# Performance work log

Measured on AMD Instinct MI355X. Metric: run time of the kernel, lower is better.

The kernel has to match this reference:

```python
import jax, jax.numpy as jnp
import numpy as np

IMG = 224          # image_size
FMAP = (56, 56)    # feature_map_dims (AdaptiveAvgPool2d((56,56)))
K_REWEIGHT = 3     # self.n_reweight
BLUR_RADIUS = 4    # KNNGaussianBlur(4): kernel 9, sigma 4


def _cdist(a, b):
    # Euclidean pairwise distance, [Na, D] x [Nb, D] -> [Na, Nb]
    a2 = jnp.sum(a * a, axis=1, keepdims=True)            # [Na,1]
    b2 = jnp.sum(b * b, axis=1, keepdims=True).T          # [1,Nb]
    d2 = a2 + b2 - 2.0 * (a @ b.T)
    return jnp.sqrt(jnp.maximum(d2, 0.0))


def _gaussian_blur(x):
    # x: [1,1,H,W]; torchvision GaussianBlur(kernel=9, sigma=4), reflect pad
    r, sigma = BLUR_RADIUS, float(BLUR_RADIUS)
    t = jnp.arange(2 * r + 1, dtype=x.dtype) - r
    g = jnp.exp(-(t * t) / (2.0 * sigma * sigma))
    g = g / jnp.sum(g)
    k2d = jnp.outer(g, g)[None, None]                     # [1,1,9,9]
    xp = jnp.pad(x, ((0, 0), (0, 0), (r, r), (r, r)), mode='reflect')
    return jax.lax.conv_general_dilated(
        xp, k2d, window_strides=(1, 1), padding='VALID',
        dimension_numbers=('NCHW', 'OIHW', 'NCHW'))


def setup_inputs() -> dict:
    key = jax.random.key(0)
    k1, k2 = jax.random.split(key)
    patch = jax.random.normal(k1, (FMAP[0] * FMAP[1], 768), dtype=jnp.float32)
    patch_lib = jax.random.normal(k2, (16384, 768), dtype=jnp.float32)
    mean = jnp.zeros((), dtype=jnp.float32)
    std = jnp.ones((), dtype=jnp.float32)
    return {"patch": patch, "patch_lib": patch_lib, "mean": mean, "std": std}


def reference(patch, patch_lib, mean, std):
    # normalization (method_name != 'Point_MAE' branch)
    p = (patch - mean) / std                               # [N, D]

    dist = _cdist(p, patch_lib)                            # [N, Nlib]
    min_val = jnp.min(dist, axis=1)                        # [N]
    min_idx = jnp.argmin(dist, axis=1)                     # [N]
    s_idx = jnp.argmax(min_val)
    s_star = jnp.max(min_val)

    m_test = p[s_idx]                                      # [D]
    m_star = patch_lib[min_idx[s_idx]]                     # [D]

    # distances of m_star to whole bank, k smallest
    w_dist = jnp.sqrt(jnp.maximum(
        jnp.sum((patch_lib - m_star) ** 2, axis=1), 0.0))  # [Nlib]
    _, nn_idx = jax.lax.top_k(-w_dist, K_REWEIGHT)         # smallest k
    m_star_knn = jnp.linalg.norm(
        m_test[None, :] - patch_lib[nn_idx[1:]], axis=1)   # [k-1]

    D_sqrt = jnp.sqrt(jnp.asarray(patch.shape[1], dtype=p.dtype))
    w = 1.0 - jnp.exp(s_star / D_sqrt) / jnp.sum(jnp.exp(m_star_knn / D_sqrt))
    s = w * s_star

    s_map = min_val.reshape(1, 1, *FMAP)
    s_map = jax.image.resize(s_map, (1, 1, IMG, IMG), method='bilinear')
    s_map = _gaussian_blur(s_map)
    return s, s_map
```

## Files before the change

kernel.cpp:

```cpp
#include <hip/hip_runtime.h>
#include <hip/hip_bf16.h>
#include <stdint.h>

#define N_PATCH 3136
#define N_PATCH_PAD 3328
#define N_LIB   16384
#define DIM     768
#define IMGSZ   224
#define FM      56

#define TILE 256
#define KT2 12
#define MT 13
#define NTILES 64

#define TAILB 64
#define D2_MARGIN 8.0f

typedef __bf16 bf16_t;
typedef __bf16 bf16x8 __attribute__((ext_vector_type(8)));
typedef __bf16 bf16x4_v __attribute__((ext_vector_type(4)));
typedef float  f32x4  __attribute__((ext_vector_type(4)));

#define FLT_MAX_ 3.402823466e+38f

#define BARF() do { asm volatile("" ::: "memory"); \
                    __builtin_amdgcn_s_barrier();  \
                    asm volatile("" ::: "memory"); } while (0)

struct Scal {
  unsigned long long approx_max_pack;
  unsigned long long cand_pack[64];
  int cand[64];
  int cand_count;
  int bar[4];
  int work;
};

__device__ __forceinline__ float wave_reduce_sum(float v) {
#pragma unroll
  for (int s = 32; s > 0; s >>= 1) v += __shfl_xor(v, s, 64);
  return v;
}

__device__ __forceinline__ float wave_reduce_min(float v) {
#pragma unroll
  for (int s = 32; s > 0; s >>= 1) v = fminf(v, __shfl_xor(v, s, 64));
  return v;
}

__device__ __forceinline__ unsigned long long shfl_xor_u64(unsigned long long v, int mask) {
  unsigned lo = (unsigned)v, hi = (unsigned)(v >> 32);
  lo = __shfl_xor(lo, mask, 64);
  hi = __shfl_xor(hi, mask, 64);
  return ((unsigned long long)hi << 32) | lo;
}

__device__ __forceinline__ void async16(const bf16_t* g, bf16_t* l) {
  __builtin_amdgcn_global_load_lds(
      (const __attribute__((address_space(1))) unsigned int*)g,
      (__attribute__((address_space(3))) unsigned int*)l, 16, 0, 0);
}

__device__ __forceinline__ void grid_bar(int* ctr, int nb) {
  __syncthreads();
  if (threadIdx.x == 0) {
    __threadfence();
    atomicAdd(ctr, 1);
    while (atomicAdd(ctr, 0) < nb) __builtin_amdgcn_s_sleep(8);
    __threadfence();
  }
  __syncthreads();
}

__device__ __forceinline__ float bf16u_to_f(unsigned short u) {
  return __uint_as_float(((unsigned)u) << 16);
}

__global__ void prep_kernel(const float* __restrict__ patch, const float* __restrict__ lib,
                            const float* __restrict__ meanp, const float* __restrict__ stdp,
                            bf16_t* __restrict__ pb, bf16_t* __restrict__ lb,
                            float* __restrict__ a2, float* __restrict__ b2, Scal* sc) {
  int t = threadIdx.x;
  int lane = t & 63;
  if (blockIdx.x == 0) {
    if (t < 64) sc->cand_pack[t] = ~0ULL;
    if (t == 64) { sc->approx_max_pack = 0ULL; sc->cand_count = 0; }
    if (t >= 65 && t < 69) sc->bar[t - 65] = 0;
    if (t == 69) sc->work = 0;
  }
  if (blockIdx.x < N_PATCH_PAD / 4) {
    int row = blockIdx.x * 4 + (t >> 6);
    if (row < N_PATCH) {
      float mu = meanp[0], sd = stdp[0];
      float acc = 0.f;
#pragma unroll
      for (int k = 0; k < 3; k++) {
        float4 v = ((const float4*)(patch + (size_t)row * DIM))[lane + 64 * k];
        v.x = (v.x - mu) / sd; v.y = (v.y - mu) / sd;
        v.z = (v.z - mu) / sd; v.w = (v.w - mu) / sd;
        bf16x4_v o = {(__bf16)v.x, (__bf16)v.y, (__bf16)v.z, (__bf16)v.w};
        *(bf16x4_v*)(pb + (size_t)row * DIM + (lane + 64 * k) * 4) = o;
        acc += v.x*v.x + v.y*v.y + v.z*v.z + v.w*v.w;
      }
      acc = wave_reduce_sum(acc);
      if (lane == 0) a2[row] = acc;
    } else {
      bf16x4_v z = {(__bf16)0.f, (__bf16)0.f, (__bf16)0.f, (__bf16)0.f};
#pragma unroll
      for (int k = 0; k < 3; k++)
        *(bf16x4_v*)(pb + (size_t)row * DIM + (lane + 64 * k) * 4) = z;
    }
  } else {
    int row = (blockIdx.x - N_PATCH_PAD / 4) * 4 + (t >> 6);
    float acc = 0.f;
#pragma unroll
    for (int k = 0; k < 3; k++) {
      float4 v = ((const float4*)(lib + (size_t)row * DIM))[lane + 64 * k];
      bf16x4_v o = {(__bf16)v.x, (__bf16)v.y, (__bf16)v.z, (__bf16)v.w};
      *(bf16x4_v*)(lb + (size_t)row * DIM + (lane + 64 * k) * 4) = o;
      acc += v.x*v.x + v.y*v.y + v.z*v.z + v.w*v.w;
    }
    acc = wave_reduce_sum(acc);
    if (lane == 0) b2[row] = acc;
  }
}

__global__ __launch_bounds__(512, 2)
void gemm_min_kernel(const bf16_t* __restrict__ pb, const bf16_t* __restrict__ lb,
                     const float* __restrict__ a2, const float* __restrict__ b2,
                     float* __restrict__ part) {
  __shared__ __align__(16) bf16_t As[2][2][128 * 64];
  __shared__ __align__(16) bf16_t Bs[2][2][128 * 64];

  const int t = threadIdx.x;
  const int wave = t >> 6;
  const int lane = t & 63;
  const int l15 = lane & 15;
  const int quad = lane >> 4;
  const int wm = (wave >> 2) * 128;
  const int wn = (wave & 3) * 64;
  const int mhw = wm >> 7;
  const int nhw = wn >> 7;
  const int wni = wn & 64;

  const int L0 = t >> 3;
  const int k0 = (t & 7) ^ (L0 & 7);
  const int sl0 = (((0 * 4 + quad) ^ (l15 & 7)) << 4);
  const int sl1 = (((1 * 4 + quad) ^ (l15 & 7)) << 4);

  const int x = blockIdx.x & 7;
  const int sblk = blockIdx.x >> 3;
  const int nt = x * 8 + (sblk & 7);
  const int n0 = nt * TILE;

  for (int g = 0; g < 4; ++g) {
    if (g * 32 + sblk >= 104) break;
    const int mt = g * 4 + (sblk >> 3);
    const int m0 = mt * TILE;

    __syncthreads();

    const bf16_t* gA = pb + (size_t)(m0 + L0) * DIM + k0 * 8;
    const bf16_t* gB = lb + (size_t)(n0 + L0) * DIM + k0 * 8;

    auto stageA = [&](int tk, int mh) {
      bf16_t* dst = &As[tk & 1][mh][0];
      const bf16_t* s = gA + (size_t)(mh * 128) * DIM + tk * 64;
      async16(s, dst + t * 8);
      async16(s + (size_t)64 * DIM, dst + 4096 + t * 8);
    };
    auto stageB = [&](int tk, int nh) {
      bf16_t* dst = &Bs[tk & 1][nh][0];
      const bf16_t* s = gB + (size_t)(nh * 128) * DIM + tk * 64;
      async16(s, dst + t * 8);
      async16(s + (size_t)64 * DIM, dst + 4096 + t * 8);
    };

    f32x4 acc[8][4];
#pragma unroll
    for (int mi = 0; mi < 8; mi++)
#pragma unroll
      for (int ni = 0; ni < 4; ni++) { f32x4 z = {0.f,0.f,0.f,0.f}; acc[mi][ni] = z; }

    bf16x8 afr[4][2], bf[2][2];

    auto readA = [&](int d, int mh) {
      const char* base = (const char*)&As[d][mhw][0];
#pragma unroll
      for (int mi = 0; mi < 4; mi++) {
        int lr = mh * 64 + mi * 16 + l15;
        afr[mi][0] = *(const bf16x8*)(base + lr * 128 + sl0);
        afr[mi][1] = *(const bf16x8*)(base + lr * 128 + sl1);
      }
    };
    auto readB = [&](int d, int nh) {
      const char* base = (const char*)&Bs[d][nhw][0];
#pragma unroll
      for (int ni = 0; ni < 2; ni++) {
        int lr = wni + nh * 32 + ni * 16 + l15;
        bf[ni][0] = *(const bf16x8*)(base + lr * 128 + sl0);
        bf[ni][1] = *(const bf16x8*)(base + lr * 128 + sl1);
      }
    };
    auto mfq = [&](int mh, int nh) {
      __builtin_amdgcn_s_setprio(1);
#pragma unroll
      for (int mi = 0; mi < 4; mi++)
#pragma unroll
        for (int ni = 0; ni < 2; ni++) {
          acc[mh*4+mi][nh*2+ni] = __builtin_amdgcn_mfma_f32_16x16x32_bf16(
              afr[mi][0], bf[ni][0], acc[mh*4+mi][nh*2+ni], 0, 0, 0);
          acc[mh*4+mi][nh*2+ni] = __builtin_amdgcn_mfma_f32_16x16x32_bf16(
              afr[mi][1], bf[ni][1], acc[mh*4+mi][nh*2+ni], 0, 0, 0);
        }
      __builtin_amdgcn_s_setprio(0);
    };

    auto half_iter = [&](int d, int tst, bool stg) {
      if (stg) {
        stageA(tst, 0);
        asm volatile("s_waitcnt vmcnt(2)" ::: "memory");
      } else {
        asm volatile("s_waitcnt vmcnt(0)" ::: "memory");
      }
      BARF();
      readB(d, 0);
      readA(d, 0);
      mfq(0, 0);
      BARF();
      readB(d, 1);
      if (stg) { stageA(tst, 1); stageB(tst, 0); }
      BARF();
      mfq(0, 1);
      BARF();
      readA(d, 1);
      if (stg) stageB(tst, 1);
      BARF();
      mfq(1, 1);
      BARF();
      readB(d, 0);
      BARF();
      mfq(1, 0);
      BARF();
    };

    stageA(0, 0); stageA(0, 1); stageB(0, 0); stageB(0, 1);

    for (int tt = 0; tt < 10; tt += 2) {
      half_iter(0, tt + 1, true);
      half_iter(1, tt + 2, true);
    }
    half_iter(0, 11, true);
    half_iter(1, 12, false);

    __syncthreads();
    unsigned* smin = (unsigned*)&As[0][0][0];
    if (t < 256) smin[t] = 0xffffffffu;
    __syncthreads();

    float b2n[4];
#pragma unroll
    for (int ni = 0; ni < 4; ni++) b2n[ni] = b2[n0 + wn + ni * 16 + l15];

#pragma unroll
    for (int mi = 0; mi < 8; mi++) {
#pragma unroll
      for (int r = 0; r < 4; r++) {
        int rloc = wm + mi * 16 + quad * 4 + r;
        int mrow = m0 + rloc;
        float a2v = a2[mrow < N_PATCH ? mrow : (N_PATCH - 1)];
        float best = a2v + b2n[0] - 2.0f * acc[mi][0][r];
#pragma unroll
        for (int ni = 1; ni < 4; ni++)
          best = fminf(best, a2v + b2n[ni] - 2.0f * acc[mi][ni][r]);
        best = fmaxf(best, 0.0f);
#pragma unroll
        for (int s = 1; s < 16; s <<= 1)
          best = fminf(best, __shfl_xor(best, s, 64));
        if (l15 == 0) atomicMin(&smin[rloc], __float_as_uint(best));
      }
    }
    __syncthreads();
    if (t < 256) part[(size_t)nt * N_PATCH_PAD + m0 + t] = __uint_as_float(smin[t]);
  }
}

__device__ __forceinline__ void wave_pick(const Scal* sc, int cnt, int lane,
                                          int* srow, float* sstar, int* ms) {
  unsigned long long pk = 0ULL;
  int rowv = 0, msv = 0;
  if (lane < cnt) {
    unsigned long long cp = sc->cand_pack[lane];
    rowv = sc->cand[lane];
    msv = (int)(cp & 0xffffffffu);
    pk = (cp & 0xffffffff00000000ULL) | (unsigned)(0xffffffffu - (unsigned)rowv);
  }
  unsigned long long m = pk;
#pragma unroll
  for (int s = 1; s < 64; s <<= 1) {
    unsigned long long o = shfl_xor_u64(m, s);
    if (o > m) m = o;
  }
  unsigned long long mask = __ballot(pk == m && lane < cnt);
  int wl = (int)(__ffsll((long long)mask) - 1);
  *srow = __shfl(rowv, wl, 64);
  *ms   = __shfl(msv, wl, 64);
  *sstar = sqrtf(__uint_as_float((unsigned)(m >> 32)));
}

__global__ __launch_bounds__(256, 2)
void tail_kernel(const float* __restrict__ part, float* __restrict__ min_val,
                 const float* __restrict__ patch, const float* __restrict__ lib,
                 const bf16_t* __restrict__ lb,
                 const float* __restrict__ meanp, const float* __restrict__ stdp,
                 Scal* __restrict__ sc, float* __restrict__ wdist2,
                 float* __restrict__ out0, float* __restrict__ outmap) {
  __shared__ union {
    unsigned long long sl[768];
    float rs[40 * 40];
  } sm;
  __shared__ float redbuf[4];
  __shared__ unsigned long long rb64[4];
  __shared__ int s_cnt;

  const int t = threadIdx.x;
  const int b = blockIdx.x;
  const int wave = t >> 6, lane = t & 63;

  {
    int row = b * 256 + t;
    unsigned long long mp = 0ULL;
    if (row < N_PATCH) {
      float m = FLT_MAX_;
#pragma unroll 8
      for (int nt = 0; nt < NTILES; nt++)
        m = fminf(m, part[(size_t)nt * N_PATCH_PAD + row]);
      float v = sqrtf(m);
      min_val[row] = v;
      mp = (((unsigned long long)__float_as_uint(v)) << 32) |
           (unsigned)(0xffffffffu - (unsigned)row);
    }
#pragma unroll
    for (int s = 1; s < 64; s <<= 1) {
      unsigned long long o = shfl_xor_u64(mp, s);
      if (o > mp) mp = o;
    }
    if (lane == 0) rb64[wave] = mp;
    __syncthreads();
    if (t == 0) {
      unsigned long long mm = rb64[0];
      if (rb64[1] > mm) mm = rb64[1];
      if (rb64[2] > mm) mm = rb64[2];
      if (rb64[3] > mm) mm = rb64[3];
      if (mm) atomicMax(&sc->approx_max_pack, mm);
    }
  }
  grid_bar(&sc->bar[0], TAILB);

  if (b == 0) {
    float amax = __uint_as_float((unsigned)(atomicMax(&sc->approx_max_pack, 0ULL) >> 32));
    for (int i = t; i < N_PATCH; i += 256) {
      if (min_val[i] >= amax - 0.05f) {
        int p = atomicAdd(&sc->cand_count, 1);
        if (p < 64) sc->cand[p] = i;
      }
    }
  }
  grid_bar(&sc->bar[1], TAILB);

  if (t == 0) s_cnt = atomicAdd(&sc->cand_count, 0);
  __syncthreads();
  int cnt = s_cnt; if (cnt > 64) cnt = 64;

  {
    float mu = meanp[0], sd = stdp[0];
    for (int c = 0; c < cnt; c++) {
      int row = sc->cand[c];
      float pv_ = (t < NTILES) ? part[(size_t)t * N_PATCH_PAD + row] : FLT_MAX_;
      pv_ = wave_reduce_min(pv_);
      if (lane == 0) redbuf[wave] = pv_;
      __syncthreads();
      float bmin = fminf(fminf(redbuf[0], redbuf[1]), fminf(redbuf[2], redbuf[3]));
      __syncthreads();

      float4 pv[3];
#pragma unroll
      for (int k = 0; k < 3; k++) {
        float4 v = ((const float4*)(patch + (size_t)row * DIM))[lane + 64 * k];
        v.x = (v.x - mu) / sd; v.y = (v.y - mu) / sd;
        v.z = (v.z - mu) / sd; v.w = (v.w - mu) / sd;
        pv[k] = v;
      }
      int nt = b;
      float pmin = part[(size_t)nt * N_PATCH_PAD + row];
      if (pmin <= bmin + D2_MARGIN) {
        unsigned long long best = ~0ULL;
        int jb = nt * 256 + wave * 64;
        for (int rr = 0; rr < 64; rr++) {
          int j = jb + rr;
          const float4* pl = (const float4*)(lib + (size_t)j * DIM);
          float acc = 0.f;
#pragma unroll
          for (int k = 0; k < 3; k++) {
            float4 l = pl[lane + 64 * k];
            float dx = pv[k].x - l.x, dy = pv[k].y - l.y;
            float dz = pv[k].z - l.z, dw = pv[k].w - l.w;
            acc += dx*dx + dy*dy + dz*dz + dw*dw;
          }
          acc = wave_reduce_sum(acc);
          unsigned long long pk = (((unsigned long long)__float_as_uint(acc)) << 32) | (unsigned)j;
          if (pk < best) best = pk;
        }
        if (lane == 0) atomicMin(&sc->cand_pack[c], best);
      }
    }
  }
  grid_bar(&sc->bar[2], TAILB);

  {
    int srow_, ms; float ss_;
    wave_pick(sc, cnt, lane, &srow_, &ss_, &ms);
    float pm[12];
    const ushort4* pms = (const ushort4*)(lb + (size_t)ms * DIM);
#pragma unroll
    for (int k = 0; k < 3; k++) {
      ushort4 u = pms[lane + 64 * k];
      pm[k*4+0] = bf16u_to_f(u.x); pm[k*4+1] = bf16u_to_f(u.y);
      pm[k*4+2] = bf16u_to_f(u.z); pm[k*4+3] = bf16u_to_f(u.w);
    }
    int jbase = b * 256 + wave * 64;
    for (int rr = 0; rr < 64; rr += 2) {
      int j0 = jbase + rr, j1 = j0 + 1;
      const ushort4* r0 = (const ushort4*)(lb + (size_t)j0 * DIM);
      const ushort4* r1 = (const ushort4*)(lb + (size_t)j1 * DIM);
      float a0 = 0.f, a1 = 0.f;
#pragma unroll
      for (int k = 0; k < 3; k++) {
        ushort4 u0 = r0[lane + 64 * k];
        ushort4 u1 = r1[lane + 64 * k];
        float d;
        d = bf16u_to_f(u0.x) - pm[k*4+0]; a0 += d * d;
        d = bf16u_to_f(u0.y) - pm[k*4+1]; a0 += d * d;
        d = bf16u_to_f(u0.z) - pm[k*4+2]; a0 += d * d;
        d = bf16u_to_f(u0.w) - pm[k*4+3]; a0 += d * d;
        d = bf16u_to_f(u1.x) - pm[k*4+0]; a1 += d * d;
        d = bf16u_to_f(u1.y) - pm[k*4+1]; a1 += d * d;
        d = bf16u_to_f(u1.z) - pm[k*4+2]; a1 += d * d;
        d = bf16u_to_f(u1.w) - pm[k*4+3]; a1 += d * d;
      }
      a0 = wave_reduce_sum(a0);
      a1 = wave_reduce_sum(a1);
      if (lane == 0) { wdist2[j0] = a0; wdist2[j1] = a1; }
    }
  }
  grid_bar(&sc->bar[3], TAILB);

  if (b == 0) {
    unsigned long long b0 = ~0ULL, b1 = ~0ULL, b2 = ~0ULL;
    for (int j = t; j < N_LIB; j += 256) {
      unsigned long long pk = (((unsigned long long)__float_as_uint(wdist2[j])) << 32) | (unsigned)j;
      if (pk < b0)      { b2 = b1; b1 = b0; b0 = pk; }
      else if (pk < b1) { b2 = b1; b1 = pk; }
      else if (pk < b2) { b2 = pk; }
    }
    sm.sl[t * 3 + 0] = b0; sm.sl[t * 3 + 1] = b1; sm.sl[t * 3 + 2] = b2;
    __syncthreads();
    if (t >= 64) return;

    unsigned long long c0 = ~0ULL, c1 = ~0ULL, c2 = ~0ULL;
#pragma unroll
    for (int e = 0; e < 12; e++) {
      unsigned long long pk = sm.sl[t * 12 + e];
      if (pk < c0)      { c2 = c1; c1 = c0; c0 = pk; }
      else if (pk < c1) { c2 = c1; c1 = pk; }
      else if (pk < c2) { c2 = pk; }
    }
    unsigned long long res1 = 0, res2 = 0;
#pragma unroll
    for (int r = 0; r < 3; r++) {
      unsigned long long m = c0;
#pragma unroll
      for (int s = 1; s < 64; s <<= 1) {
        unsigned long long o = shfl_xor_u64(m, s);
        if (o < m) m = o;
      }
      if (r == 1) res1 = m;
      if (r == 2) res2 = m;
      if (c0 == m) { c0 = c1; c1 = c2; c2 = ~0ULL; }
    }
    int nA = (int)(res1 & 0xffffffffu);
    int nB = (int)(res2 & 0xffffffffu);

    int srow, ms2; float sstar;
    wave_pick(sc, cnt, t, &srow, &sstar, &ms2);

    float mu = meanp[0], sd = stdp[0];
    float accA = 0.f, accB = 0.f;
#pragma unroll
    for (int k = 0; k < 3; k++) {
      float4 p4 = ((const float4*)(patch + (size_t)srow * DIM))[t + 64 * k];
      float4 a4 = ((const float4*)(lib + (size_t)nA * DIM))[t + 64 * k];
      float4 b4 = ((const float4*)(lib + (size_t)nB * DIM))[t + 64 * k];
      float px = (p4.x - mu) / sd, py = (p4.y - mu) / sd;
      float pz = (p4.z - mu) / sd, pw = (p4.w - mu) / sd;
      float dax = px - a4.x, day = py - a4.y, daz = pz - a4.z, daw = pw - a4.w;
      float dbx = px - b4.x, dby = py - b4.y, dbz = pz - b4.z, dbw = pw - b4.w;
      accA += dax*dax + day*day + daz*daz + daw*daw;
      accB += dbx*dbx + dby*dby + dbz*dbz + dbw*dbw;
    }
    accA = wave_reduce_sum(accA);
    accB = wave_reduce_sum(accB);
    if (t == 0) {
      float dsq = sqrtf((float)DIM);
      float d1 = sqrtf(accA), d2v = sqrtf(accB);
      float w = 1.0f - expf(sstar / dsq) / (expf(d1 / dsq) + expf(d2v / dsq));
      out0[0] = w * sstar;
    }
    return;
  }

  if (b > 49) return;
  {
    int tile = b - 1;
    int bx = tile % 7, by = tile / 7;
    int ox0 = bx * 32, oy0 = by * 32;

    for (int i = t; i < 1600; i += 256) {
      int ly = i / 40, lx = i % 40;
      int gy = oy0 - 4 + ly; gy = gy < 0 ? 0 : (gy > 223 ? 223 : gy);
      int gx = ox0 - 4 + lx; gx = gx < 0 ? 0 : (gx > 223 ? 223 : gx);
      float sy = fminf(fmaxf(0.25f * gy - 0.375f, 0.0f), 55.0f);
      float sx = fminf(fmaxf(0.25f * gx - 0.375f, 0.0f), 55.0f);
      int y0 = (int)sy; if (y0 > 54) y0 = 54;
      int x0 = (int)sx; if (x0 > 54) x0 = 54;
      float fy = sy - y0, fx = sx - x0;
      float v00 = min_val[y0*FM + x0],     v01 = min_val[y0*FM + x0 + 1];
      float v10 = min_val[(y0+1)*FM + x0], v11 = min_val[(y0+1)*FM + x0 + 1];
      float a = v00 + fx * (v01 - v00);
      float bb = v10 + fx * (v11 - v10);
      sm.rs[i] = a + fy * (bb - a);
    }
    __syncthreads();

    float g[9]; float gs = 0.f;
#pragma unroll
    for (int i = 0; i < 9; i++) { float tt = (float)(i - 4); g[i] = expf(-(tt*tt)/32.0f); gs += g[i]; }
#pragma unroll
    for (int i = 0; i < 9; i++) g[i] /= gs;

    for (int p = t; p < 1024; p += 256) {
      int y = oy0 + p / 32, x = ox0 + (p & 31);
      float acc = 0.f;
#pragma unroll
      for (int dy = 0; dy < 9; dy++) {
        int yy = y + dy - 4;
        yy = yy < 0 ? -yy : (yy > IMGSZ - 1 ? 2*(IMGSZ-1) - yy : yy);
        int lyy = yy - (oy0 - 4);
        float ra = 0.f;
#pragma unroll
        for (int dx = 0; dx < 9; dx++) {
          int xx = x + dx - 4;
          xx = xx < 0 ? -xx : (xx > IMGSZ - 1 ? 2*(IMGSZ-1) - xx : xx);
          ra += g[dx] * sm.rs[lyy * 40 + (xx - (ox0 - 4))];
        }
        acc += g[dy] * ra;
      }
      outmap[y * IMGSZ + x] = acc;
    }
  }
}

extern "C" void kernel_launch(void* const* d_in, const int* in_sizes, int n_in,
                              void* d_out, int out_size, void* d_ws, size_t ws_size,
                              hipStream_t stream) {
  const float* patch = (const float*)d_in[0];
  const float* lib   = (const float*)d_in[1];
  const float* meanp = (const float*)d_in[2];
  const float* stdp  = (const float*)d_in[3];
  float* out = (float*)d_out;

  char* ws = (char*)d_ws;
  size_t off = 0;
  auto alloc = [&](size_t bytes) -> void* {
    void* p = ws + off;
    off = (off + bytes + 255) & ~(size_t)255;
    return p;
  };
  bf16_t* pb      = (bf16_t*)alloc((size_t)N_PATCH_PAD * DIM * sizeof(bf16_t));
  bf16_t* lb      = (bf16_t*)alloc((size_t)N_LIB * DIM * sizeof(bf16_t));
  float* a2       = (float*)alloc(N_PATCH * sizeof(float));
  float* b2       = (float*)alloc(N_LIB * sizeof(float));
  float* part     = (float*)alloc((size_t)N_PATCH_PAD * NTILES * sizeof(float));
  float* min_val  = (float*)alloc(N_PATCH * sizeof(float));
  float* wdist2   = (float*)alloc(N_LIB * sizeof(float));
  Scal*  sc       = (Scal*)alloc(sizeof(Scal));

  prep_kernel<<<N_PATCH_PAD / 4 + N_LIB / 4, 256, 0, stream>>>(patch, lib, meanp, stdp,
                                                               pb, lb, a2, b2, sc);
  gemm_min_kernel<<<256, 512, 0, stream>>>(pb, lb, a2, b2, part);
  tail_kernel<<<TAILB, 256, 0, stream>>>(part, min_val, patch, lib, lb, meanp, stdp,
                                         sc, wdist2, out, out + 1);
}
```

Measured before the change: 329.5 us.

## Simplify GEMM main loop to one-barrier double buffering and transpose partial-min layout

Replaces the fine-grained interleaved half-iteration schedule, which had many barriers and staged A/B halves between MFMA quarters, with a simple loop. Each k-tile now does a full wait and one barrier, issues the next tile's async loads, then computes the whole tile with B fragments held in registers. The per-tile partial minimum buffer is transposed to row-major [row][tile], so the tail reduction reads 64 contiguous values per row with one wave per row. The full vmcnt(0) wait per iteration may expose more load latency than the old staggered schedule did, and holding more fragments in registers raises register pressure.

```diff
diff --git a/kernel.cpp b/kernel.cpp
--- a/kernel.cpp
+++ b/kernel.cpp
@@ -23,10 +23,6 @@
 typedef float  f32x4  __attribute__((ext_vector_type(4)));
 
 #define FLT_MAX_ 3.402823466e+38f
-
-#define BARF() do { asm volatile("" ::: "memory"); \
-                    __builtin_amdgcn_s_barrier();  \
-                    asm volatile("" ::: "memory"); } while (0)
 
 struct Scal {
   unsigned long long approx_max_pack;
@@ -164,95 +160,70 @@
     const bf16_t* gA = pb + (size_t)(m0 + L0) * DIM + k0 * 8;
     const bf16_t* gB = lb + (size_t)(n0 + L0) * DIM + k0 * 8;
 
-    auto stageA = [&](int tk, int mh) {
-      bf16_t* dst = &As[tk & 1][mh][0];
-      const bf16_t* s = gA + (size_t)(mh * 128) * DIM + tk * 64;
-      async16(s, dst + t * 8);
-      async16(s + (size_t)64 * DIM, dst + 4096 + t * 8);
+    auto stageT = [&](int tk) {
+      bf16_t* dA0 = &As[tk & 1][0][0];
+      bf16_t* dA1 = &As[tk & 1][1][0];
+      bf16_t* dB0 = &Bs[tk & 1][0][0];
+      bf16_t* dB1 = &Bs[tk & 1][1][0];
+      const bf16_t* sA = gA + tk * 64;
+      const bf16_t* sB = gB + tk * 64;
+      async16(sA,                       dA0 + t * 8);
+      async16(sA + (size_t)64  * DIM,   dA0 + 4096 + t * 8);
+      async16(sA + (size_t)128 * DIM,   dA1 + t * 8);
+      async16(sA + (size_t)192 * DIM,   dA1 + 4096 + t * 8);
+      async16(sB,                       dB0 + t * 8);
+      async16(sB + (size_t)64  * DIM,   dB0 + 4096 + t * 8);
+      async16(sB + (size_t)128 * DIM,   dB1 + t * 8);
+      async16(sB + (size_t)192 * DIM,   dB1 + 4096 + t * 8);
     };
-    auto stageB = [&](int tk, int nh) {
-      bf16_t* dst = &Bs[tk & 1][nh][0];
-      const bf16_t* s = gB + (size_t)(nh * 128) * DIM + tk * 64;
-      async16(s, dst + t * 8);
-      async16(s + (size_t)64 * DIM, dst + 4096 + t * 8);
+
+    f32x4 acc[8][4];
+#pragma unroll
+    for (int mi = 0; mi < 8; mi++)
+#pragma unroll
+      for (int ni = 0; ni < 4; ni++) { f32x4 z = {0.f,0.f,0.f,0.f}; acc[mi][ni] = z; }
+
+    auto computeTile = [&](int d) {
+      const char* Ab = (const char*)&As[d][mhw][0];
+      const char* Bb = (const char*)&Bs[d][nhw][0];
+      bf16x8 bfr[4][2];
+#pragma unroll
+      for (int ni = 0; ni < 4; ni++) {
+        int lr = wni + ni * 16 + l15;
+        bfr[ni][0] = *(const bf16x8*)(Bb + lr * 128 + sl0);
+        bfr[ni][1] = *(const bf16x8*)(Bb + lr * 128 + sl1);
+      }
+#pragma unroll
+      for (int q = 0; q < 4; q++) {
+        bf16x8 aq[2][2];
+#pragma unroll
+        for (int mi = 0; mi < 2; mi++) {
+          int lr = q * 32 + mi * 16 + l15;
+          aq[mi][0] = *(const bf16x8*)(Ab + lr * 128 + sl0);
+          aq[mi][1] = *(const bf16x8*)(Ab + lr * 128 + sl1);
+        }
+        __builtin_amdgcn_s_setprio(1);
+#pragma unroll
+        for (int mi = 0; mi < 2; mi++)
+#pragma unroll
+          for (int ni = 0; ni < 4; ni++) {
+            acc[q*2+mi][ni] = __builtin_amdgcn_mfma_f32_16x16x32_bf16(
+                aq[mi][0], bfr[ni][0], acc[q*2+mi][ni], 0, 0, 0);
+            acc[q*2+mi][ni] = __builtin_amdgcn_mfma_f32_16x16x32_bf16(
+                aq[mi][1], bfr[ni][1], acc[q*2+mi][ni], 0, 0, 0);
+          }
+        __builtin_amdgcn_s_setprio(0);
+      }
     };
 
-    f32x4 acc[8][4];
-#pragma unroll
-    for (int mi = 0; mi < 8; mi++)
-#pragma unroll
-      for (int ni = 0; ni < 4; ni++) { f32x4 z = {0.f,0.f,0.f,0.f}; acc[mi][ni] = z; }
-
-    bf16x8 afr[4][2], bf[2][2];
-
-    auto readA = [&](int d, int mh) {
-      const char* base = (const char*)&As[d][mhw][0];
-#pragma unroll
-      for (int mi = 0; mi < 4; mi++) {
-        int lr = mh * 64 + mi * 16 + l15;
-        afr[mi][0] = *(const bf16x8*)(base + lr * 128 + sl0);
-        afr[mi][1] = *(const bf16x8*)(base + lr * 128 + sl1);
-      }
-    };
-    auto readB = [&](int d, int nh) {
-      const char* base = (const char*)&Bs[d][nhw][0];
-#pragma unroll
-      for (int ni = 0; ni < 2; ni++) {
-        int lr = wni + nh * 32 + ni * 16 + l15;
-        bf[ni][0] = *(const bf16x8*)(base + lr * 128 + sl0);
-        bf[ni][1] = *(const bf16x8*)(base + lr * 128 + sl1);
-      }
-    };
-    auto mfq = [&](int mh, int nh) {
-      __builtin_amdgcn_s_setprio(1);
-#pragma unroll
-      for (int mi = 0; mi < 4; mi++)
-#pragma unroll
-        for (int ni = 0; ni < 2; ni++) {
-          acc[mh*4+mi][nh*2+ni] = __builtin_amdgcn_mfma_f32_16x16x32_bf16(
-              afr[mi][0], bf[ni][0], acc[mh*4+mi][nh*2+ni], 0, 0, 0);
-          acc[mh*4+mi][nh*2+ni] = __builtin_amdgcn_mfma_f32_16x16x32_bf16(
-              afr[mi][1], bf[ni][1], acc[mh*4+mi][nh*2+ni], 0, 0, 0);
-        }
-      __builtin_amdgcn_s_setprio(0);
-    };
-
-    auto half_iter = [&](int d, int tst, bool stg) {
-      if (stg) {
-        stageA(tst, 0);
-        asm volatile("s_waitcnt vmcnt(2)" ::: "memory");
-      } else {
-        asm volatile("s_waitcnt vmcnt(0)" ::: "memory");
-      }
-      BARF();
-      readB(d, 0);
-      readA(d, 0);
-      mfq(0, 0);
-      BARF();
-      readB(d, 1);
-      if (stg) { stageA(tst, 1); stageB(tst, 0); }
-      BARF();
-      mfq(0, 1);
-      BARF();
-      readA(d, 1);
-      if (stg) stageB(tst, 1);
-      BARF();
-      mfq(1, 1);
-      BARF();
-      readB(d, 0);
-      BARF();
-      mfq(1, 0);
-      BARF();
-    };
-
-    stageA(0, 0); stageA(0, 1); stageB(0, 0); stageB(0, 1);
-
-    for (int tt = 0; tt < 10; tt += 2) {
-      half_iter(0, tt + 1, true);
-      half_iter(1, tt + 2, true);
-    }
-    half_iter(0, 11, true);
-    half_iter(1, 12, false);
+    stageT(0);
+    for (int tk = 0; tk < KT2; ++tk) {
+      asm volatile("s_waitcnt vmcnt(0) lgkmcnt(0)" ::: "memory");
+      __builtin_amdgcn_s_barrier();
+      asm volatile("" ::: "memory");
+      if (tk + 1 < KT2) stageT(tk + 1);
+      computeTile(tk & 1);
+    }
 
     __syncthreads();
     unsigned* smin = (unsigned*)&As[0][0][0];
@@ -282,7 +253,7 @@
       }
     }
     __syncthreads();
-    if (t < 256) part[(size_t)nt * N_PATCH_PAD + m0 + t] = __uint_as_float(smin[t]);
+    if (t < 256) part[(size_t)(m0 + t) * NTILES + nt] = __uint_as_float(smin[t]);
   }
 }
 
@@ -329,22 +300,19 @@
   const int wave = t >> 6, lane = t & 63;
 
   {
-    int row = b * 256 + t;
     unsigned long long mp = 0ULL;
-    if (row < N_PATCH) {
-      float m = FLT_MAX_;
-#pragma unroll 8
-      for (int nt = 0; nt < NTILES; nt++)
-        m = fminf(m, part[(size_t)nt * N_PATCH_PAD + row]);
-      float v = sqrtf(m);
-      min_val[row] = v;
-      mp = (((unsigned long long)__float_as_uint(v)) << 32) |
-           (unsigned)(0xffffffffu - (unsigned)row);
-    }
-#pragma unroll
-    for (int s = 1; s < 64; s <<= 1) {
-      unsigned long long o = shfl_xor_u64(mp, s);
-      if (o > mp) mp = o;
+    for (int i = wave; i < 256; i += 4) {
+      int row = b * 256 + i;
+      if (row >= N_PATCH) break;
+      float v = part[(size_t)row * NTILES + lane];
+      v = wave_reduce_min(v);
+      if (lane == 0) {
+        float sv = sqrtf(v);
+        min_val[row] = sv;
+        unsigned long long cand = (((unsigned long long)__float_as_uint(sv)) << 32) |
+                                  (unsigned)(0xffffffffu - (unsigned)row);
+        if (cand > mp) mp = cand;
+      }
     }
     if (lane == 0) rb64[wave] = mp;
     __syncthreads();
@@ -377,7 +345,7 @@
     float mu = meanp[0], sd = stdp[0];
     for (int c = 0; c < cnt; c++) {
       int row = sc->cand[c];
-      float pv_ = (t < NTILES) ? part[(size_t)t * N_PATCH_PAD + row] : FLT_MAX_;
+      float pv_ = (t < NTILES) ? part[(size_t)row * NTILES + t] : FLT_MAX_;
       pv_ = wave_reduce_min(pv_);
       if (lane == 0) redbuf[wave] = pv_;
       __syncthreads();
@@ -393,7 +361,7 @@
         pv[k] = v;
       }
       int nt = b;
-      float pmin = part[(size_t)nt * N_PATCH_PAD + row];
+      float pmin = part[(size_t)row * NTILES + nt];
       if (pmin <= bmin + D2_MARGIN) {
         unsigned long long best = ~0ULL;
         int jb = nt * 256 + wave * 64;
```

New measurement: 349.7 us. 6.1% more time.
